# Optimization experiments

Measured on AMD Instinct MI355X. Metric: run time of the kernel, lower is better.

## Reference

```python
import jax, jax.numpy as jnp
import numpy as np

T, B, I, H = 2048, 32, 512, 512


def setup_inputs() -> dict:
    key = jax.random.key(0)
    ks = jax.random.split(key, 8)
    s = 1.0 / np.sqrt(H)
    return {
        "X": jax.random.normal(ks[0], (T, B, I), dtype=jnp.float32),
        "h": jax.random.normal(ks[1], (B, H), dtype=jnp.float32),
        "W_ih": jax.random.uniform(ks[2], (3 * H, I), jnp.float32, -s, s),
        "W_hh": jax.random.uniform(ks[3], (3 * H, H), jnp.float32, -s, s),
        "b_ih": jax.random.uniform(ks[4], (3 * H,), jnp.float32, -s, s),
        "b_hh": jax.random.uniform(ks[5], (3 * H,), jnp.float32, -s, s),
        "W_dense": jax.random.uniform(ks[6], (H, I), jnp.float32, -s, s),
        "b_dense": jax.random.uniform(ks[7], (H,), jnp.float32, -s, s),
    }


def reference(X, h, W_ih, W_hh, b_ih, b_hh, W_dense, b_dense):
    # Precompute input-side gate projections for all timesteps: [T, B, 3H]
    gi_all = jnp.einsum('tbi,gi->tbg', X, W_ih) + b_ih

    def step(h, gi):
        # hidden-side gates for this step: [B, 3H]
        gh = h @ W_hh.T + b_hh
        i_r, i_z, i_n = jnp.split(gi, 3, axis=-1)
        h_r, h_z, h_n = jnp.split(gh, 3, axis=-1)
        r = jax.nn.sigmoid(i_r + h_r)
        z = jax.nn.sigmoid(i_z + h_z)
        n = jnp.tanh(i_n + r * h_n)
        h_new = (1.0 - z) * n + z * h
        return h_new, h_new

    h_last, outputs = jax.lax.scan(step, h, gi_all)
    # AddNorm with dropout=0 (eval): dense(X) + outputs
    dense = jnp.einsum('tbi,hi->tbh', X, W_dense) + b_dense
    return outputs + dense, h_last
```

## Files before the change

### kernel.cpp

```cpp
#include <hip/hip_runtime.h>

#define TT   2048
#define NB   32
#define NI   512
#define NHID 512
#define NWG  32
#define KSL  16

typedef float    f32x4 __attribute__((ext_vector_type(4)));
typedef _Float16 f16x8 __attribute__((ext_vector_type(8)));

__device__ __align__(256) unsigned int g_flags[576];
__device__ __align__(256) _Float16    g_hb0[NB * NHID];
__device__ __align__(256) _Float16    g_hb1[NB * NHID];
__device__ __align__(256) _Float16    g_wfrag[NWG][4][16][64][8];

__device__ __forceinline__ f16x8 pack8(f32x4 a, f32x4 b) {
    f16x8 r;
    r[0] = (_Float16)a[0]; r[1] = (_Float16)a[1]; r[2] = (_Float16)a[2]; r[3] = (_Float16)a[3];
    r[4] = (_Float16)b[0]; r[5] = (_Float16)b[1]; r[6] = (_Float16)b[2]; r[7] = (_Float16)b[3];
    return r;
}

__device__ __forceinline__ unsigned int poll_load_nt(const unsigned int* p) {
    unsigned int v;
    asm volatile("global_load_dword %0, %1, off nt\n\ts_waitcnt vmcnt(0)"
                 : "=v"(v) : "v"(p) : "memory");
    return v;
}

extern "C" __global__ void init_flags_k() {
    for (int i = threadIdx.x; i < 576; i += 256) g_flags[i] = 0u;
}

extern "C" __global__ void pack_wfrag_k(const float* __restrict__ Wih,
                                        const float* __restrict__ Wd) {
    const int w    = blockIdx.x;
    const int tid  = threadIdx.x;
    const int lane = tid & 63;
    const int mat  = tid >> 6;
    const int r15  = lane & 15;
    const int g4   = lane >> 4;
    const float* src = (mat < 3) ? (Wih + (size_t)(mat * 512 + w * KSL + r15) * NI)
                                 : (Wd  + (size_t)(w * KSL + r15) * NI);
    #pragma unroll
    for (int kc = 0; kc < 16; ++kc) {
        const f32x4* p = (const f32x4*)(src + kc * 32 + g4 * 8);
        *(f16x8*)&g_wfrag[w][mat][kc][lane][0] = pack8(p[0], p[1]);
    }
}

extern "C" __global__ void __launch_bounds__(256, 1)
gru_persist(const float* __restrict__ X, const float* __restrict__ h0,
            const float* __restrict__ Wih, const float* __restrict__ Whh,
            const float* __restrict__ bih, const float* __restrict__ bhh,
            const float* __restrict__ Wd,  const float* __restrict__ bd,
            float* __restrict__ out)
{
    if (blockIdx.x >= 256) {
        __builtin_amdgcn_s_setprio(0);
        unsigned int* done = g_flags + 514;
        float s0 = 1.0f + (float)threadIdx.x, s1 = s0 + .1f, s2 = s0 + .2f, s3 = s0 + .3f;
        float s4 = s0 + .4f, s5 = s0 + .5f, s6 = s0 + .6f, s7 = s0 + .7f;
        const float mm = 1.0000001f, cc = 1.0e-7f;
        while (__hip_atomic_load(done, __ATOMIC_RELAXED,
                                 __HIP_MEMORY_SCOPE_AGENT) < 64u) {
            #pragma unroll 32
            for (int i = 0; i < 2048; ++i) {
                s0 = __builtin_fmaf(s0, mm, cc); s1 = __builtin_fmaf(s1, mm, cc);
                s2 = __builtin_fmaf(s2, mm, cc); s3 = __builtin_fmaf(s3, mm, cc);
                s4 = __builtin_fmaf(s4, mm, cc); s5 = __builtin_fmaf(s5, mm, cc);
                s6 = __builtin_fmaf(s6, mm, cc); s7 = __builtin_fmaf(s7, mm, cc);
            }
        }
        asm volatile("" :: "v"(s0), "v"(s1), "v"(s2), "v"(s3),
                          "v"(s4), "v"(s5), "v"(s6), "v"(s7));
        return;
    }
    if (blockIdx.x & 7) return;
    const int w  = blockIdx.x >> 3;
    const int ks = w * KSL;

    __shared__ _Float16 fragWhh[3][16][64][8];
    __shared__ float    gi_lds[2][2][4][16][20];
    __shared__ float    bias_h[3][KSL];
    __shared__ float    bias_i[4][KSL];
    __shared__ unsigned int seq[8];
    __shared__ unsigned int fast_sh;
    volatile unsigned int* vseq = seq;

    const int tid  = threadIdx.x;
    const int lane = tid & 63;
    const int wv   = tid >> 6;
    const int half = wv & 1;
    const int isp  = wv >> 1;
    const int r15  = lane & 15;
    const int g4   = lane >> 4;

    if (tid < 8) seq[tid] = 0u;
    if (tid < KSL) {
        int k = ks + tid;
        bias_h[0][tid] = bhh[k];
        bias_h[1][tid] = bhh[512 + k];
        bias_h[2][tid] = bhh[1024 + k];
        bias_i[0][tid] = bih[k];
        bias_i[1][tid] = bih[512 + k];
        bias_i[2][tid] = bih[1024 + k];
        bias_i[3][tid] = bd[k];
    }
    for (int s = wv; s < 3; s += 4) {
        const float* src = Whh + (size_t)(s * 512 + ks + r15) * NHID;
        #pragma unroll
        for (int kc = 0; kc < 16; ++kc) {
            const f32x4* p = (const f32x4*)(src + kc * 32 + g4 * 8);
            *(f16x8*)&fragWhh[s][kc][lane][0] = pack8(p[0], p[1]);
        }
    }
    if (tid == 0) {
        unsigned int xcc;
        asm volatile("s_getreg_b32 %0, hwreg(HW_REG_XCC_ID, 0, 32)" : "=s"(xcc));
        unsigned int bit = 1u << (xcc & 7);
        unsigned int* mask  = g_flags + 512;
        unsigned int* count = g_flags + 513;
        unsigned int old = __hip_atomic_fetch_or(mask, bit, __ATOMIC_RELAXED,
                                                 __HIP_MEMORY_SCOPE_AGENT);
        asm volatile("" :: "v"(old));
        __hip_atomic_fetch_add(count, 1u, __ATOMIC_RELAXED, __HIP_MEMORY_SCOPE_AGENT);
        while (__hip_atomic_load(count, __ATOMIC_RELAXED,
                                 __HIP_MEMORY_SCOPE_AGENT) < NWG) { }
        unsigned int m = __hip_atomic_load(mask, __ATOMIC_RELAXED,
                                           __HIP_MEMORY_SCOPE_AGENT);
        fast_sh = ((m & (m - 1)) == 0) ? 1u : 0u;
    }
    __syncthreads();
    const bool fast = (fast_sh != 0);
    const int  bg   = half * 16 + r15;

    if (!isp) {
        __builtin_amdgcn_s_setprio(1);
        f32x4 hold = *(const f32x4*)(h0 + (size_t)bg * NHID + ks + g4 * 4);
        const f32x4 bhr = *(const f32x4*)&bias_h[0][g4 * 4];
        const f32x4 bhz = *(const f32x4*)&bias_h[1][g4 * 4];
        const f32x4 bhn = *(const f32x4*)&bias_h[2][g4 * 4];
        const f32x4 bir = *(const f32x4*)&bias_i[0][g4 * 4];
        const f32x4 biz = *(const f32x4*)&bias_i[1][g4 * 4];
        const f32x4 bin = *(const f32x4*)&bias_i[2][g4 * 4];
        const f32x4 bd4 = *(const f32x4*)&bias_i[3][g4 * 4];
        const float* h0row = h0 + (size_t)bg * NHID;

        #pragma unroll 1
        for (int t = 0; t < TT; ++t) {
            if (t > 0 && lane < NWG) {
                const unsigned int* fp = &g_flags[lane * 16 + half * 8];
                if (fast) { while (poll_load_nt(fp) < (unsigned)t) { } }
                else      { while (__hip_atomic_load(fp, __ATOMIC_RELAXED,
                                       __HIP_MEMORY_SCOPE_AGENT) < (unsigned)t) { } }
            }
            f16x8 Bf[16];
            if (t == 0) {
                #pragma unroll
                for (int kc = 0; kc < 16; ++kc) {
                    const f32x4* p = (const f32x4*)(h0row + kc * 32 + g4 * 8);
                    Bf[kc] = pack8(p[0], p[1]);
                }
            } else {
                const _Float16* hrow = ((t & 1) ? g_hb1 : g_hb0) + (size_t)bg * NHID;
                if (fast) {
                    #pragma unroll
                    for (int kc = 0; kc < 16; ++kc) {
                        const _Float16* p = hrow + kc * 32 + g4 * 8;
                        asm volatile("global_load_dwordx4 %0, %1, off nt"
                                     : "=v"(Bf[kc]) : "v"(p));
                    }
                } else {
                    #pragma unroll
                    for (int kc = 0; kc < 16; ++kc) {
                        const _Float16* p = hrow + kc * 32 + g4 * 8;
                        asm volatile("global_load_dwordx4 %0, %1, off sc0 sc1"
                                     : "=v"(Bf[kc]) : "v"(p));
                    }
                }
                asm volatile("s_waitcnt vmcnt(0)" ::: "memory");
                __builtin_amdgcn_sched_barrier(0);
            }
            f32x4 a0 = {0.f,0.f,0.f,0.f}, a1 = a0, a2 = a0;
            #pragma unroll
            for (int kc = 0; kc < 16; ++kc) {
                f16x8 w0 = *(const f16x8*)&fragWhh[0][kc][lane][0];
                f16x8 w1 = *(const f16x8*)&fragWhh[1][kc][lane][0];
                f16x8 w2 = *(const f16x8*)&fragWhh[2][kc][lane][0];
                a0 = __builtin_amdgcn_mfma_f32_16x16x32_f16(w0, Bf[kc], a0, 0, 0, 0);
                a1 = __builtin_amdgcn_mfma_f32_16x16x32_f16(w1, Bf[kc], a1, 0, 0, 0);
                a2 = __builtin_amdgcn_mfma_f32_16x16x32_f16(w2, Bf[kc], a2, 0, 0, 0);
            }
            while (vseq[half] < (unsigned)(t + 1)) { }
            const int par = t & 1;
            f32x4 gr = *(const f32x4*)&gi_lds[par][half][0][r15][g4 * 4];
            f32x4 gz = *(const f32x4*)&gi_lds[par][half][1][r15][g4 * 4];
            f32x4 gn = *(const f32x4*)&gi_lds[par][half][2][r15][g4 * 4];
            f32x4 gd = *(const f32x4*)&gi_lds[par][half][3][r15][g4 * 4];
            asm volatile("s_waitcnt lgkmcnt(0)" ::: "memory");
            if (lane == 0) vseq[2 + half] = (unsigned)(t + 1);
            f32x4 hn, o;
            #pragma unroll
            for (int i = 0; i < 4; ++i) {
                float rr = 1.f / (1.f + __expf(-((gr[i] + bir[i]) + (a0[i] + bhr[i]))));
                float zz = 1.f / (1.f + __expf(-((gz[i] + biz[i]) + (a1[i] + bhz[i]))));
                float aa = (gn[i] + bin[i]) + rr * (a2[i] + bhn[i]);
                float nn = 1.f - 2.f / (__expf(2.f * aa) + 1.f);
                hn[i] = (1.f - zz) * nn + zz * hold[i];
                o[i]  = hn[i] + gd[i] + bd4[i];
            }
            hold = hn;
            union { _Float16 h[4]; unsigned long long u; } cv;
            cv.h[0] = (_Float16)hn[0]; cv.h[1] = (_Float16)hn[1];
            cv.h[2] = (_Float16)hn[2]; cv.h[3] = (_Float16)hn[3];
            _Float16* hw = (((t + 1) & 1) ? g_hb1 : g_hb0) + (size_t)bg * NHID + ks + g4 * 4;
            if (fast) {
                *(unsigned long long*)hw = cv.u;
            } else {
                asm volatile("global_store_dwordx2 %0, %1, off sc0 sc1"
                             :: "v"(hw), "v"(cv.u) : "memory");
            }
            asm volatile("s_waitcnt vmcnt(0)" ::: "memory");
            if (lane == 0) {
                unsigned int* fp = &g_flags[w * 16 + half * 8];
                if (fast) *(volatile unsigned int*)fp = (unsigned)(t + 1);
                else __hip_atomic_store(fp, (unsigned)(t + 1), __ATOMIC_RELAXED,
                                        __HIP_MEMORY_SCOPE_AGENT);
            }
            *(f32x4*)(out + (size_t)t * (NB * NHID) + (size_t)bg * NHID + ks + g4 * 4) = o;
        }
        *(f32x4*)(out + (size_t)TT * (NB * NHID) + (size_t)bg * NHID + ks + g4 * 4) = hold;
        if (lane == 0)
            __hip_atomic_fetch_add(g_flags + 514, 1u, __ATOMIC_RELAXED,
                                   __HIP_MEMORY_SCOPE_AGENT);
    } else {
        __builtin_amdgcn_s_setprio(1);
        const float* Xrow = X + (size_t)bg * NI;

        #pragma unroll 1
        for (int tp = 0; tp < TT; ++tp) {
            while ((int)vseq[2 + half] < tp - 1) { }
            const float* xp = Xrow + (size_t)tp * (NB * NI);
            f16x8 Bf[16];
            #pragma unroll
            for (int kc = 0; kc < 16; ++kc) {
                const f32x4* p = (const f32x4*)(xp + kc * 32 + g4 * 8);
                Bf[kc] = pack8(p[0], p[1]);
            }
            f32x4 acc[4];
            #pragma unroll
            for (int q = 0; q < 4; ++q) acc[q] = (f32x4){0.f, 0.f, 0.f, 0.f};
            #pragma unroll
            for (int mat = 0; mat < 4; ++mat) {
                f16x8 wb[16];
                #pragma unroll
                for (int kc = 0; kc < 16; ++kc)
                    wb[kc] = *(const f16x8*)&g_wfrag[w][mat][kc][lane][0];
                #pragma unroll
                for (int kc = 0; kc < 16; ++kc)
                    acc[mat] = __builtin_amdgcn_mfma_f32_16x16x32_f16(wb[kc], Bf[kc], acc[mat], 0, 0, 0);
            }
            const int par = tp & 1;
            *(f32x4*)&gi_lds[par][half][0][r15][g4 * 4] = acc[0];
            *(f32x4*)&gi_lds[par][half][1][r15][g4 * 4] = acc[1];
            *(f32x4*)&gi_lds[par][half][2][r15][g4 * 4] = acc[2];
            *(f32x4*)&gi_lds[par][half][3][r15][g4 * 4] = acc[3];
            asm volatile("s_waitcnt lgkmcnt(0)" ::: "memory");
            if (lane == 0) vseq[half] = (unsigned)(tp + 1);
        }
    }
}

extern "C" void kernel_launch(void* const* d_in, const int* in_sizes, int n_in,
                              void* d_out, int out_size, void* d_ws, size_t ws_size,
                              hipStream_t stream) {
    const float* X   = (const float*)d_in[0];
    const float* h0  = (const float*)d_in[1];
    const float* Wih = (const float*)d_in[2];
    const float* Whh = (const float*)d_in[3];
    const float* bih = (const float*)d_in[4];
    const float* bhh = (const float*)d_in[5];
    const float* Wd  = (const float*)d_in[6];
    const float* bd  = (const float*)d_in[7];
    float* out = (float*)d_out;

    init_flags_k<<<dim3(1), dim3(256), 0, stream>>>();
    pack_wfrag_k<<<dim3(NWG), dim3(256), 0, stream>>>(Wih, Wd);

    gru_persist<<<dim3(512), dim3(256), 0, stream>>>(
        X, h0, Wih, Whh, bih, bhh, Wd, bd, out);
}
```

Before: 10.25 ms.

## Split recurrent gate matmuls across three wave pairs and replace burner blocks with in-wave spin work

Each workgroup now has 512 threads. Six waves compute the r, z and n hidden-gate MFMAs in parallel, one gate per wave pair, and the z and n partials go through LDS to the wave that runs the GRU update. The goal is to shorten the serial per-timestep recurrent matmul chain, and each gate's chain uses two accumulators to expose more MFMA parallelism. The separate filler blocks that burned FMAs to keep clocks up are removed. Waiting waves now burn FMAs inside their spin loops instead, which adds intra-block LDS synchronization and may contend for issue slots.

```diff
diff --git a/kernel.cpp b/kernel.cpp
--- a/kernel.cpp
+++ b/kernel.cpp
@@ -50,54 +50,38 @@
     }
 }
 
-extern "C" __global__ void __launch_bounds__(256, 1)
+#define BURN48(b0,b1,b2,bm,bc) { _Pragma("unroll") \
+    for (int ii_ = 0; ii_ < 16; ++ii_) { \
+        b0 = __builtin_fmaf(b0, bm, bc); b1 = __builtin_fmaf(b1, bm, bc); \
+        b2 = __builtin_fmaf(b2, bm, bc); } }
+
+extern "C" __global__ void __launch_bounds__(512, 1)
 gru_persist(const float* __restrict__ X, const float* __restrict__ h0,
             const float* __restrict__ Wih, const float* __restrict__ Whh,
             const float* __restrict__ bih, const float* __restrict__ bhh,
             const float* __restrict__ Wd,  const float* __restrict__ bd,
             float* __restrict__ out)
 {
-    if (blockIdx.x >= 256) {
-        __builtin_amdgcn_s_setprio(0);
-        unsigned int* done = g_flags + 514;
-        float s0 = 1.0f + (float)threadIdx.x, s1 = s0 + .1f, s2 = s0 + .2f, s3 = s0 + .3f;
-        float s4 = s0 + .4f, s5 = s0 + .5f, s6 = s0 + .6f, s7 = s0 + .7f;
-        const float mm = 1.0000001f, cc = 1.0e-7f;
-        while (__hip_atomic_load(done, __ATOMIC_RELAXED,
-                                 __HIP_MEMORY_SCOPE_AGENT) < 64u) {
-            #pragma unroll 32
-            for (int i = 0; i < 2048; ++i) {
-                s0 = __builtin_fmaf(s0, mm, cc); s1 = __builtin_fmaf(s1, mm, cc);
-                s2 = __builtin_fmaf(s2, mm, cc); s3 = __builtin_fmaf(s3, mm, cc);
-                s4 = __builtin_fmaf(s4, mm, cc); s5 = __builtin_fmaf(s5, mm, cc);
-                s6 = __builtin_fmaf(s6, mm, cc); s7 = __builtin_fmaf(s7, mm, cc);
-            }
-        }
-        asm volatile("" :: "v"(s0), "v"(s1), "v"(s2), "v"(s3),
-                          "v"(s4), "v"(s5), "v"(s6), "v"(s7));
-        return;
-    }
     if (blockIdx.x & 7) return;
     const int w  = blockIdx.x >> 3;
     const int ks = w * KSL;
 
     __shared__ _Float16 fragWhh[3][16][64][8];
     __shared__ float    gi_lds[2][2][4][16][20];
+    __shared__ f32x4    gh_part[2][2][64];
     __shared__ float    bias_h[3][KSL];
     __shared__ float    bias_i[4][KSL];
-    __shared__ unsigned int seq[8];
+    __shared__ unsigned int seq[16];
     __shared__ unsigned int fast_sh;
     volatile unsigned int* vseq = seq;
 
     const int tid  = threadIdx.x;
     const int lane = tid & 63;
     const int wv   = tid >> 6;
-    const int half = wv & 1;
-    const int isp  = wv >> 1;
     const int r15  = lane & 15;
     const int g4   = lane >> 4;
 
-    if (tid < 8) seq[tid] = 0u;
+    if (tid < 16) seq[tid] = 0u;
     if (tid < KSL) {
         int k = ks + tid;
         bias_h[0][tid] = bhh[k];
@@ -108,12 +92,12 @@
         bias_i[2][tid] = bih[1024 + k];
         bias_i[3][tid] = bd[k];
     }
-    for (int s = wv; s < 3; s += 4) {
-        const float* src = Whh + (size_t)(s * 512 + ks + r15) * NHID;
+    if (wv < 3) {
+        const float* src = Whh + (size_t)(wv * 512 + ks + r15) * NHID;
         #pragma unroll
         for (int kc = 0; kc < 16; ++kc) {
             const f32x4* p = (const f32x4*)(src + kc * 32 + g4 * 8);
-            *(f16x8*)&fragWhh[s][kc][lane][0] = pack8(p[0], p[1]);
+            *(f16x8*)&fragWhh[wv][kc][lane][0] = pack8(p[0], p[1]);
         }
     }
     if (tid == 0) {
@@ -134,27 +118,46 @@
     }
     __syncthreads();
     const bool fast = (fast_sh != 0);
-    const int  bg   = half * 16 + r15;
-
-    if (!isp) {
+
+    float b0 = 1.0f + 0.5f * (float)tid, b1 = b0 + 0.3f, b2 = b0 + 0.7f;
+    const float bm = 1.0000001f, bc = 1.0e-7f;
+
+    if (wv < 6) {
+        const int g  = wv >> 1;
+        const int hf = wv & 1;
+        const int bg = hf * 16 + r15;
         __builtin_amdgcn_s_setprio(1);
-        f32x4 hold = *(const f32x4*)(h0 + (size_t)bg * NHID + ks + g4 * 4);
-        const f32x4 bhr = *(const f32x4*)&bias_h[0][g4 * 4];
-        const f32x4 bhz = *(const f32x4*)&bias_h[1][g4 * 4];
-        const f32x4 bhn = *(const f32x4*)&bias_h[2][g4 * 4];
-        const f32x4 bir = *(const f32x4*)&bias_i[0][g4 * 4];
-        const f32x4 biz = *(const f32x4*)&bias_i[1][g4 * 4];
-        const f32x4 bin = *(const f32x4*)&bias_i[2][g4 * 4];
-        const f32x4 bd4 = *(const f32x4*)&bias_i[3][g4 * 4];
+
+        f32x4 hold;
+        f32x4 bhr, bhz, bhn, bir, biz, bin, bd4;
+        if (g == 0) {
+            hold = *(const f32x4*)(h0 + (size_t)bg * NHID + ks + g4 * 4);
+            bhr = *(const f32x4*)&bias_h[0][g4 * 4];
+            bhz = *(const f32x4*)&bias_h[1][g4 * 4];
+            bhn = *(const f32x4*)&bias_h[2][g4 * 4];
+            bir = *(const f32x4*)&bias_i[0][g4 * 4];
+            biz = *(const f32x4*)&bias_i[1][g4 * 4];
+            bin = *(const f32x4*)&bias_i[2][g4 * 4];
+            bd4 = *(const f32x4*)&bias_i[3][g4 * 4];
+        }
         const float* h0row = h0 + (size_t)bg * NHID;
 
         #pragma unroll 1
         for (int t = 0; t < TT; ++t) {
-            if (t > 0 && lane < NWG) {
-                const unsigned int* fp = &g_flags[lane * 16 + half * 8];
-                if (fast) { while (poll_load_nt(fp) < (unsigned)t) { } }
-                else      { while (__hip_atomic_load(fp, __ATOMIC_RELAXED,
-                                       __HIP_MEMORY_SCOPE_AGENT) < (unsigned)t) { } }
+            if (t > 0) {
+                const unsigned int* fp = &g_flags[lane * 16 + hf * 8];
+                for (;;) {
+                    int rdy = 1;
+                    if (lane < NWG) {
+                        unsigned v = fast ? poll_load_nt(fp)
+                                          : __hip_atomic_load(fp, __ATOMIC_RELAXED,
+                                                              __HIP_MEMORY_SCOPE_AGENT);
+                        rdy = (v >= (unsigned)t);
+                    }
+                    if (__all(rdy)) break;
+                    BURN48(b0, b1, b2, bm, bc);
+                }
+                asm volatile("" ::: "memory");
             }
             f16x8 Bf[16];
             if (t == 0) {
@@ -183,30 +186,45 @@
                 asm volatile("s_waitcnt vmcnt(0)" ::: "memory");
                 __builtin_amdgcn_sched_barrier(0);
             }
-            f32x4 a0 = {0.f,0.f,0.f,0.f}, a1 = a0, a2 = a0;
-            #pragma unroll
-            for (int kc = 0; kc < 16; ++kc) {
-                f16x8 w0 = *(const f16x8*)&fragWhh[0][kc][lane][0];
-                f16x8 w1 = *(const f16x8*)&fragWhh[1][kc][lane][0];
-                f16x8 w2 = *(const f16x8*)&fragWhh[2][kc][lane][0];
-                a0 = __builtin_amdgcn_mfma_f32_16x16x32_f16(w0, Bf[kc], a0, 0, 0, 0);
-                a1 = __builtin_amdgcn_mfma_f32_16x16x32_f16(w1, Bf[kc], a1, 0, 0, 0);
-                a2 = __builtin_amdgcn_mfma_f32_16x16x32_f16(w2, Bf[kc], a2, 0, 0, 0);
-            }
-            while (vseq[half] < (unsigned)(t + 1)) { }
+            f32x4 aA = {0.f,0.f,0.f,0.f}, aB = aA;
+            #pragma unroll
+            for (int kc = 0; kc < 16; kc += 2) {
+                f16x8 w0 = *(const f16x8*)&fragWhh[g][kc][lane][0];
+                f16x8 w1 = *(const f16x8*)&fragWhh[g][kc + 1][lane][0];
+                aA = __builtin_amdgcn_mfma_f32_16x16x32_f16(w0, Bf[kc],     aA, 0, 0, 0);
+                aB = __builtin_amdgcn_mfma_f32_16x16x32_f16(w1, Bf[kc + 1], aB, 0, 0, 0);
+            }
+            f32x4 acc;
+            #pragma unroll
+            for (int i = 0; i < 4; ++i) acc[i] = aA[i] + aB[i];
+
+            if (g > 0) {
+                gh_part[g - 1][hf][lane] = acc;
+                asm volatile("s_waitcnt lgkmcnt(0)" ::: "memory");
+                if (lane == 0) vseq[4 + (g - 1) * 2 + hf] = (unsigned)(t + 1);
+                continue;
+            }
+            while (vseq[4 + hf] < (unsigned)(t + 1) ||
+                   vseq[6 + hf] < (unsigned)(t + 1)) { }
+            asm volatile("" ::: "memory");
+            f32x4 az = gh_part[0][hf][lane];
+            f32x4 an = gh_part[1][hf][lane];
+            while (vseq[hf] < (unsigned)(t + 1)) { }
+            asm volatile("" ::: "memory");
             const int par = t & 1;
-            f32x4 gr = *(const f32x4*)&gi_lds[par][half][0][r15][g4 * 4];
-            f32x4 gz = *(const f32x4*)&gi_lds[par][half][1][r15][g4 * 4];
-            f32x4 gn = *(const f32x4*)&gi_lds[par][half][2][r15][g4 * 4];
-            f32x4 gd = *(const f32x4*)&gi_lds[par][half][3][r15][g4 * 4];
+            f32x4 gr = *(const f32x4*)&gi_lds[par][hf][0][r15][g4 * 4];
+            f32x4 gz = *(const f32x4*)&gi_lds[par][hf][1][r15][g4 * 4];
+            f32x4 gn = *(const f32x4*)&gi_lds[par][hf][2][r15][g4 * 4];
+            f32x4 gd = *(const f32x4*)&gi_lds[par][hf][3][r15][g4 * 4];
             asm volatile("s_waitcnt lgkmcnt(0)" ::: "memory");
-            if (lane == 0) vseq[2 + half] = (unsigned)(t + 1);
+            if (lane == 0) vseq[2 + hf] = (unsigned)(t + 1);
+
             f32x4 hn, o;
             #pragma unroll
             for (int i = 0; i < 4; ++i) {
-                float rr = 1.f / (1.f + __expf(-((gr[i] + bir[i]) + (a0[i] + bhr[i]))));
-                float zz = 1.f / (1.f + __expf(-((gz[i] + biz[i]) + (a1[i] + bhz[i]))));
-                float aa = (gn[i] + bin[i]) + rr * (a2[i] + bhn[i]);
+                float rr = 1.f / (1.f + __expf(-((gr[i] + bir[i]) + (acc[i] + bhr[i]))));
+                float zz = 1.f / (1.f + __expf(-((gz[i] + biz[i]) + (az[i] + bhz[i]))));
+                float aa = (gn[i] + bin[i]) + rr * (an[i] + bhn[i]);
                 float nn = 1.f - 2.f / (__expf(2.f * aa) + 1.f);
                 hn[i] = (1.f - zz) * nn + zz * hold[i];
                 o[i]  = hn[i] + gd[i] + bd4[i];
@@ -224,24 +242,26 @@
             }
             asm volatile("s_waitcnt vmcnt(0)" ::: "memory");
             if (lane == 0) {
-                unsigned int* fp = &g_flags[w * 16 + half * 8];
+                unsigned int* fp = &g_flags[w * 16 + hf * 8];
                 if (fast) *(volatile unsigned int*)fp = (unsigned)(t + 1);
                 else __hip_atomic_store(fp, (unsigned)(t + 1), __ATOMIC_RELAXED,
                                         __HIP_MEMORY_SCOPE_AGENT);
             }
             *(f32x4*)(out + (size_t)t * (NB * NHID) + (size_t)bg * NHID + ks + g4 * 4) = o;
         }
-        *(f32x4*)(out + (size_t)TT * (NB * NHID) + (size_t)bg * NHID + ks + g4 * 4) = hold;
-        if (lane == 0)
-            __hip_atomic_fetch_add(g_flags + 514, 1u, __ATOMIC_RELAXED,
-                                   __HIP_MEMORY_SCOPE_AGENT);
+        if (g == 0)
+            *(f32x4*)(out + (size_t)TT * (NB * NHID) + (size_t)bg * NHID + ks + g4 * 4) = hold;
+        asm volatile("" :: "v"(b0), "v"(b1), "v"(b2));
     } else {
+        const int hf = wv & 1;
+        const int bg = hf * 16 + r15;
         __builtin_amdgcn_s_setprio(1);
         const float* Xrow = X + (size_t)bg * NI;
 
         #pragma unroll 1
         for (int tp = 0; tp < TT; ++tp) {
-            while ((int)vseq[2 + half] < tp - 1) { }
+            while ((int)vseq[2 + hf] < tp - 1) { BURN48(b0, b1, b2, bm, bc); }
+            asm volatile("" ::: "memory");
             const float* xp = Xrow + (size_t)tp * (NB * NI);
             f16x8 Bf[16];
             #pragma unroll
@@ -263,13 +283,14 @@
                     acc[mat] = __builtin_amdgcn_mfma_f32_16x16x32_f16(wb[kc], Bf[kc], acc[mat], 0, 0, 0);
             }
             const int par = tp & 1;
-            *(f32x4*)&gi_lds[par][half][0][r15][g4 * 4] = acc[0];
-            *(f32x4*)&gi_lds[par][half][1][r15][g4 * 4] = acc[1];
-            *(f32x4*)&gi_lds[par][half][2][r15][g4 * 4] = acc[2];
-            *(f32x4*)&gi_lds[par][half][3][r15][g4 * 4] = acc[3];
+            *(f32x4*)&gi_lds[par][hf][0][r15][g4 * 4] = acc[0];
+            *(f32x4*)&gi_lds[par][hf][1][r15][g4 * 4] = acc[1];
+            *(f32x4*)&gi_lds[par][hf][2][r15][g4 * 4] = acc[2];
+            *(f32x4*)&gi_lds[par][hf][3][r15][g4 * 4] = acc[3];
             asm volatile("s_waitcnt lgkmcnt(0)" ::: "memory");
-            if (lane == 0) vseq[half] = (unsigned)(tp + 1);
+            if (lane == 0) vseq[hf] = (unsigned)(tp + 1);
         }
+        asm volatile("" :: "v"(b0), "v"(b1), "v"(b2));
     }
 }
 
@@ -289,6 +310,6 @@
     init_flags_k<<<dim3(1), dim3(256), 0, stream>>>();
     pack_wfrag_k<<<dim3(NWG), dim3(256), 0, stream>>>(Wih, Wd);
 
-    gru_persist<<<dim3(512), dim3(256), 0, stream>>>(
+    gru_persist<<<dim3(256), dim3(512), 0, stream>>>(
         X, h0, Wih, Whh, bih, bhh, Wd, bd, out);
 }
```

Measured after the change: 23.87 ms. 133% more time.
